# Kernel optimization log

Measured on AMD Instinct MI355X. Metric: run time of the kernel, lower is better.

The kernel has to match this reference:

```python
import jax, jax.numpy as jnp
import numpy as np

# Fixed production-scale dims (equal-size graphs -> no ragged padding needed)
B, NPG, C, H, L, FFN, NC = 16, 512, 128, 8, 4, 512, 4
D = C // H          # head dim = 16
T = NPG + 1         # +1 virtual graph token
EPG = 8192          # edges per graph (avg degree 16)
E = B * EPG


def _ln(x, g, b, eps=1e-5):
    m = x.mean(-1, keepdims=True)
    v = ((x - m) ** 2).mean(-1, keepdims=True)
    return (x - m) * jax.lax.rsqrt(v + eps) * g + b


def setup_inputs() -> dict:
    key = jax.random.key(0)
    ks = jax.random.split(key, 24)
    N = B * NPG
    node_feats = jax.random.normal(ks[0], (N, 3), jnp.float32)
    # intra-graph edges: local endpoints + per-graph node offset (matches batch_ptr math)
    local = jax.random.randint(ks[1], (2, B, EPG), 0, NPG)
    offs = (jnp.arange(B) * NPG)[None, :, None]
    edge_index = (local + offs).reshape(2, E)
    edge_attr = jax.random.randint(ks[2], (E,), 0, 10)

    def nrm(k, shape, scale=0.02):
        return jax.random.normal(k, shape, jnp.float32) * scale

    params = {
        "W_node": nrm(ks[3], (3, C), 0.3), "b_node": jnp.zeros((C,), jnp.float32),
        "graph_token": nrm(ks[4], (C,), 1.0),
        "edge_bias_table": nrm(ks[5], (11, H), 0.1).at[0].set(0.0),  # padding_idx=0
        "in_deg_emb": nrm(ks[6], (512, C)).at[0].set(0.0),           # padding_idx=0
        "out_deg_emb": nrm(ks[7], (512, C)).at[0].set(0.0),
        "vnode_bias": nrm(ks[8], (H,), 1.0),
        "Wq": nrm(ks[9], (L, C, C)), "bq": jnp.zeros((L, C), jnp.float32),
        "Wk": nrm(ks[10], (L, C, C)), "bk": jnp.zeros((L, C), jnp.float32),
        "Wv": nrm(ks[11], (L, C, C)), "bv": jnp.zeros((L, C), jnp.float32),
        "Wo": nrm(ks[12], (L, C, C)), "bo": jnp.zeros((L, C), jnp.float32),
        "ln1_g": jnp.ones((L, C), jnp.float32), "ln1_b": jnp.zeros((L, C), jnp.float32),
        "ln2_g": jnp.ones((L, C), jnp.float32), "ln2_b": jnp.zeros((L, C), jnp.float32),
        "W1": nrm(ks[13], (L, C, FFN)), "b1": jnp.zeros((L, FFN), jnp.float32),
        "W2": nrm(ks[14], (L, FFN, C)), "b2": jnp.zeros((L, C), jnp.float32),
        "normf_g": jnp.ones((C,), jnp.float32), "normf_b": jnp.zeros((C,), jnp.float32),
        "Wc1": nrm(ks[15], (C, C // 2)), "bc1": jnp.zeros((C // 2,), jnp.float32),
        "Wc2": nrm(ks[16], (C // 2, NC)), "bc2": jnp.zeros((NC,), jnp.float32),
    }
    return {"node_feats": node_feats, "edge_index": edge_index,
            "edge_attr": edge_attr, "num_graphs": B, **params}


def reference(node_feats, W_node, b_node, graph_token, edge_bias_table,
              in_deg_emb, out_deg_emb, vnode_bias,
              Wq, bq, Wk, bk, Wv, bv, Wo, bo,
              ln1_g, ln1_b, ln2_g, ln2_b, W1, b1, W2, b2,
              normf_g, normf_b, Wc1, bc1, Wc2, bc2,
              edge_index, edge_attr, num_graphs):
    N = node_feats.shape[0]
    npg = N // num_graphs
    t = npg + 1
    src, dst = edge_index[0], edge_index[1]
    # degree encoders (scatter_add of ones == segment_sum)
    in_deg = jnp.clip(jax.ops.segment_sum(jnp.ones_like(dst), dst, num_segments=N), 0, 511)
    out_deg = jnp.clip(jax.ops.segment_sum(jnp.ones_like(src), src, num_segments=N), 0, 511)
    x_enc = node_feats @ W_node + b_node + in_deg_emb[in_deg] + out_deg_emb[out_deg]
    # equal-size graphs with sorted batch ids -> padding loop is a reshape, mask all-False
    x = jnp.concatenate(
        [jnp.broadcast_to(graph_token, (num_graphs, 1, C)),
         x_enc.reshape(num_graphs, npg, C)], axis=1)  # [B, T, C]
    # attention bias: vnode row/col + scattered edge-attr embeddings
    bias = jnp.zeros((num_graphs, H, t, t), jnp.float32)
    bias = bias.at[:, :, 0, :].set(vnode_bias[None, :, None])
    bias = bias.at[:, :, :, 0].set(vnode_bias[None, :, None])
    eb = edge_bias_table[jnp.clip(edge_attr, 0, 9) + 1]  # [E, H]
    g = src // npg
    sl = src - g * npg + 1
    dl = dst - g * npg + 1
    bias = bias.at[g, :, sl, dl].add(eb)  # duplicate edges accumulate (scatter_add)
    scale = 1.0 / np.sqrt(D).astype(np.float32)
    for l in range(L):  # key_padding_mask is all-False here -> masked_fill is a no-op
        h = _ln(x, ln1_g[l], ln1_b[l])
        q = (h @ Wq[l] + bq[l]).reshape(num_graphs, t, H, D)
        k = (h @ Wk[l] + bk[l]).reshape(num_graphs, t, H, D)
        v = (h @ Wv[l] + bv[l]).reshape(num_graphs, t, H, D)
        scores = jnp.einsum('bthd,bshd->bhts', q, k) * scale + bias
        attn = jax.nn.softmax(scores, axis=-1)
        o = jnp.einsum('bhts,bshd->bthd', attn, v).reshape(num_graphs, t, C)
        x = x + o @ Wo[l] + bo[l]
        h2 = _ln(x, ln2_g[l], ln2_b[l])
        x = x + jax.nn.gelu(h2 @ W1[l] + b1[l], approximate=False) @ W2[l] + b2[l]
    x = _ln(x, normf_g, normf_b)
    gr = x[:, 0, :]  # virtual-node readout
    return jax.nn.gelu(gr @ Wc1 + bc1, approximate=False) @ Wc2 + bc2
```

## Files before the change

### kernel.cpp

```cpp
#include <hip/hip_runtime.h>
#include <hip/hip_bf16.h>

#define BB 16
#define NPG 512
#define CC 128
#define HH 8
#define LL 4
#define FFN 512
#define NCLS 4
#define DD 16
#define TT 513
#define EE 131072
#define NNODES 8192
#define ROWS (BB * TT)
#define ECAP 64
#define SP 544
#define BSTR 292

static constexpr size_t XROWS = (size_t)BB * TT;
static constexpr size_t XSZ   = XROWS * CC;
static constexpr size_t VTSZ  = (size_t)BB * HH * DD * SP;

typedef unsigned short ushort_t;
typedef __attribute__((ext_vector_type(8))) short short8;
typedef __attribute__((ext_vector_type(4))) float floatx4;

__device__ __forceinline__ float gelu_exact(float v) {
    return 0.5f * v * (1.0f + erff(v * 0.70710678118654752440f));
}
__device__ __forceinline__ ushort_t f2bf(float f) {
    union { float f; unsigned u; } c; c.f = f;
    unsigned u = c.u;
    return (ushort_t)((u + 0x7FFFu + ((u >> 16) & 1u)) >> 16);
}
__device__ __forceinline__ int swz(int row, int col, int stride) {
    int kb = col >> 3;
    return row * stride + (((kb ^ (row & 7)) << 3) | (col & 7));
}

__device__ __forceinline__ void qkv_stage(const ushort_t* hs,
                                          const ushort_t* Wtq, const float* bq_,
                                          const ushort_t* Wtk, const float* bk_,
                                          const ushort_t* Wtv, const float* bv_,
                                          ushort_t* qb, ushort_t* kb, ushort_t* vt,
                                          int m0, int wave, int lq, int quad) {
    const short* hsS = (const short*)hs;
    int n0 = wave * 32;
    int c0 = n0 + lq, c1 = n0 + 16 + lq;
    const short* Ws[3] = {(const short*)Wtq, (const short*)Wtk, (const short*)Wtv};
    const float* bs[3] = {bq_, bk_, bv_};
    size_t rB0 = (size_t)(n0 + lq) * CC, rB1 = (size_t)(n0 + 16 + lq) * CC;

    #pragma unroll
    for (int m = 0; m < 3; ++m) {
        const short* W = Ws[m];
        floatx4 a0 = {0.f,0.f,0.f,0.f}, a1 = a0;
        #pragma unroll
        for (int k0 = 0; k0 < CC; k0 += 32) {
            short8 af = *(const short8*)(hsS + swz(lq, k0 + quad * 8, 128));
            short8 b0 = *(const short8*)(W + rB0 + k0 + quad * 8);
            short8 b1 = *(const short8*)(W + rB1 + k0 + quad * 8);
            a0 = __builtin_amdgcn_mfma_f32_16x16x32_bf16(af, b0, a0, 0, 0, 0);
            a1 = __builtin_amdgcn_mfma_f32_16x16x32_bf16(af, b1, a1, 0, 0, 0);
        }
        float bv0 = bs[m][c0], bv1 = bs[m][c1];
        #pragma unroll
        for (int rg = 0; rg < 4; ++rg) {
            int r = m0 + quad * 4 + rg;
            float v0 = a0[rg] + bv0;
            float v1 = a1[rg] + bv1;
            if (m == 0) {
                qb[(size_t)r * CC + c0] = f2bf(v0 * 0.25f);
                qb[(size_t)r * CC + c1] = f2bf(v1 * 0.25f);
            } else if (m == 1) {
                kb[(size_t)r * CC + c0] = f2bf(v0);
                kb[(size_t)r * CC + c1] = f2bf(v1);
            } else {
                int bg = r / TT;
                int s = r - bg * TT;
                vt[((size_t)(bg * HH + (c0 >> 4)) * DD + (c0 & 15)) * SP + s] = f2bf(v0);
                vt[((size_t)(bg * HH + (c1 >> 4)) * DD + (c1 & 15)) * SP + s] = f2bf(v1);
            }
        }
    }
}

__global__ __launch_bounds__(256) void deg_csr_kernel(const int* __restrict__ ei,
                                                      const int* __restrict__ ea,
                                                      int* __restrict__ deg_in,
                                                      int* __restrict__ deg_out,
                                                      int* __restrict__ cnt,
                                                      int* __restrict__ ebuf) {
    int e = blockIdx.x * 256 + threadIdx.x;
    if (e >= EE) return;
    int src = ei[e], dst = ei[EE + e];
    atomicAdd(&deg_out[src], 1);
    atomicAdd(&deg_in[dst], 1);
    int g = src >> 9;
    int sl = src - (g << 9) + 1;
    int dl = dst - (g << 9) + 1;
    int a = ea[e];
    a = (a < 0) ? 0 : (a > 9 ? 9 : a);
    a += 1;
    int row = g * TT + sl;
    int pos = atomicAdd(&cnt[row], 1);
    if (pos < ECAP) ebuf[(size_t)row * ECAP + pos] = dl | (a << 16);
}

__global__ __launch_bounds__(256) void encode_kernel(const float* __restrict__ nf,
                                                     const float* __restrict__ Wn,
                                                     const float* __restrict__ bn,
                                                     const float* __restrict__ gt,
                                                     const float* __restrict__ ide,
                                                     const float* __restrict__ ode,
                                                     const int* __restrict__ deg_in,
                                                     const int* __restrict__ deg_out,
                                                     float* __restrict__ x) {
    int gid = blockIdx.x * 256 + threadIdx.x;
    if (gid >= (int)(XROWS * CC)) return;
    int c = gid & (CC - 1);
    int row = gid >> 7;
    int b = row / TT;
    int t = row - b * TT;
    float val;
    if (t == 0) {
        val = gt[c];
    } else {
        int i = b * NPG + t - 1;
        val = bn[c] + nf[i*3+0]*Wn[0*CC + c] + nf[i*3+1]*Wn[1*CC + c] + nf[i*3+2]*Wn[2*CC + c];
        int di = min(deg_in[i], 511);
        int dq = min(deg_out[i], 511);
        val += ide[(size_t)di * CC + c] + ode[(size_t)dq * CC + c];
    }
    x[(size_t)row * CC + c] = val;
}

struct TrDesc {
    const float* src[24];
    ushort_t*    dst[24];
    int          K[24];
    int          N[24];
};
__global__ __launch_bounds__(256) void tr_kernel(TrDesc d) {
    int z = blockIdx.z;
    int K = d.K[z], N = d.N[z];
    int tilesN = N >> 6;
    int ntile = (K >> 6) * tilesN;
    int tile = blockIdx.x;
    if (tile >= ntile) return;
    int k0 = (tile / tilesN) << 6;
    int n0 = (tile - (tile / tilesN) * tilesN) << 6;
    const float* src = d.src[z];
    ushort_t* dst = d.dst[z];
    __shared__ float t[64][65];
    int tid = threadIdx.x;
    int c = tid & 63, rb = tid >> 6;
    #pragma unroll
    for (int kk = 0; kk < 64; kk += 4)
        t[kk + rb][c] = src[(size_t)(k0 + kk + rb) * N + n0 + c];
    __syncthreads();
    #pragma unroll
    for (int nn = 0; nn < 64; nn += 4)
        dst[(size_t)(n0 + nn + rb) * K + k0 + c] = f2bf(t[c][nn + rb]);
}

__global__ __launch_bounds__(256) void pre_kernel(const float* __restrict__ x_,
                                                  const float* __restrict__ ln1g_,
                                                  const float* __restrict__ ln1b_,
                                                  const ushort_t* __restrict__ Wtq,
                                                  const float* __restrict__ bq_,
                                                  const ushort_t* __restrict__ Wtk,
                                                  const float* __restrict__ bk_,
                                                  const ushort_t* __restrict__ Wtv,
                                                  const float* __restrict__ bv_,
                                                  ushort_t* __restrict__ qb,
                                                  ushort_t* __restrict__ kb,
                                                  ushort_t* __restrict__ vt) {
    int m0 = blockIdx.x * 16;
    int tid = threadIdx.x;
    int wave = tid >> 6, lane = tid & 63, lq = lane & 15, quad = lane >> 4;

    __shared__ ushort_t hs[16 * 128];
    __shared__ float sred[4][16][2];

    int n0 = wave * 32;
    int c0 = n0 + lq, c1 = n0 + 16 + lq;
    float w0[4], w1[4];
    #pragma unroll
    for (int rg = 0; rg < 4; ++rg) {
        int r = m0 + quad * 4 + rg;
        w0[rg] = x_[(size_t)r * CC + c0];
        w1[rg] = x_[(size_t)r * CC + c1];
    }
    #pragma unroll
    for (int rg = 0; rg < 4; ++rg) {
        float s1 = w0[rg] + w1[rg];
        float s2 = w0[rg]*w0[rg] + w1[rg]*w1[rg];
        #pragma unroll
        for (int m = 1; m < 16; m <<= 1) {
            s1 += __shfl_xor(s1, m, 64);
            s2 += __shfl_xor(s2, m, 64);
        }
        if (lq == 0) { sred[wave][quad*4+rg][0] = s1; sred[wave][quad*4+rg][1] = s2; }
    }
    __syncthreads();
    float g0 = ln1g_[c0], g1 = ln1g_[c1], lb0 = ln1b_[c0], lb1 = ln1b_[c1];
    #pragma unroll
    for (int rg = 0; rg < 4; ++rg) {
        int row = quad * 4 + rg;
        float S1 = sred[0][row][0] + sred[1][row][0] + sred[2][row][0] + sred[3][row][0];
        float S2 = sred[0][row][1] + sred[1][row][1] + sred[2][row][1] + sred[3][row][1];
        float mn = S1 * (1.0f/CC);
        float var = S2 * (1.0f/CC) - mn * mn;
        float rs = rsqrtf(var + 1e-5f);
        hs[swz(row, c0, 128)] = f2bf((w0[rg] - mn) * rs * g0 + lb0);
        hs[swz(row, c1, 128)] = f2bf((w1[rg] - mn) * rs * g1 + lb1);
    }
    __syncthreads();
    qkv_stage(hs, Wtq, bq_, Wtk, bk_, Wtv, bv_, qb, kb, vt, m0, wave, lq, quad);
}

__global__ __launch_bounds__(256) void mega_kernel(const ushort_t* __restrict__ obf,
                                                   const ushort_t* __restrict__ WtO,
                                                   const float* __restrict__ bo_,
                                                   const float* __restrict__ ln2g_,
                                                   const float* __restrict__ ln2b_,
                                                   const ushort_t* __restrict__ Wt1_,
                                                   const float* __restrict__ b1_,
                                                   const ushort_t* __restrict__ Wt2_,
                                                   const float* __restrict__ b2_,
                                                   const float* __restrict__ ln1g_,
                                                   const float* __restrict__ ln1b_,
                                                   const ushort_t* __restrict__ Wtq,
                                                   const float* __restrict__ bq_,
                                                   const ushort_t* __restrict__ Wtk,
                                                   const float* __restrict__ bk_,
                                                   const ushort_t* __restrict__ Wtv,
                                                   const float* __restrict__ bv_,
                                                   float* __restrict__ x_,
                                                   ushort_t* __restrict__ qb,
                                                   ushort_t* __restrict__ kb,
                                                   ushort_t* __restrict__ vt,
                                                   int doQKV) {
    int m0 = blockIdx.x * 16;
    int tid = threadIdx.x;
    int wave = tid >> 6, lane = tid & 63, lq = lane & 15, quad = lane >> 4;

    __shared__ ushort_t hs[16 * 128];
    __shared__ ushort_t ms[16 * 512];
    __shared__ float sred[4][16][2];

    int n0 = wave * 32;
    int c0 = n0 + lq, c1 = n0 + 16 + lq;
    float vv0[4], vv1[4];

    {
        const short* Ab = (const short*)obf;
        const short* W = (const short*)WtO;
        size_t rowA = (size_t)(m0 + lq) * CC;
        size_t rB0 = (size_t)(n0 + lq) * CC, rB1 = (size_t)(n0 + 16 + lq) * CC;
        floatx4 a0 = {0.f,0.f,0.f,0.f}, a1 = a0;
        #pragma unroll
        for (int k0 = 0; k0 < CC; k0 += 32) {
            short8 af = *(const short8*)(Ab + rowA + k0 + quad * 8);
            short8 b0 = *(const short8*)(W + rB0 + k0 + quad * 8);
            short8 b1 = *(const short8*)(W + rB1 + k0 + quad * 8);
            a0 = __builtin_amdgcn_mfma_f32_16x16x32_bf16(af, b0, a0, 0, 0, 0);
            a1 = __builtin_amdgcn_mfma_f32_16x16x32_bf16(af, b1, a1, 0, 0, 0);
        }
        float bv0 = bo_[c0], bv1 = bo_[c1];
        #pragma unroll
        for (int rg = 0; rg < 4; ++rg) {
            int r = m0 + quad * 4 + rg;
            vv0[rg] = a0[rg] + bv0 + x_[(size_t)r * CC + c0];
            vv1[rg] = a1[rg] + bv1 + x_[(size_t)r * CC + c1];
        }
        #pragma unroll
        for (int rg = 0; rg < 4; ++rg) {
            float s1 = vv0[rg] + vv1[rg];
            float s2 = vv0[rg]*vv0[rg] + vv1[rg]*vv1[rg];
            #pragma unroll
            for (int m = 1; m < 16; m <<= 1) {
                s1 += __shfl_xor(s1, m, 64);
                s2 += __shfl_xor(s2, m, 64);
            }
            if (lq == 0) { sred[wave][quad*4+rg][0] = s1; sred[wave][quad*4+rg][1] = s2; }
        }
        __syncthreads();
        float g0 = ln2g_[c0], g1 = ln2g_[c1], lb0 = ln2b_[c0], lb1 = ln2b_[c1];
        #pragma unroll
        for (int rg = 0; rg < 4; ++rg) {
            int row = quad * 4 + rg;
            float S1 = sred[0][row][0] + sred[1][row][0] + sred[2][row][0] + sred[3][row][0];
            float S2 = sred[0][row][1] + sred[1][row][1] + sred[2][row][1] + sred[3][row][1];
            float mn = S1 * (1.0f/CC);
            float var = S2 * (1.0f/CC) - mn * mn;
            float rs = rsqrtf(var + 1e-5f);
            hs[swz(row, c0, 128)] = f2bf((vv0[rg] - mn) * rs * g0 + lb0);
            hs[swz(row, c1, 128)] = f2bf((vv1[rg] - mn) * rs * g1 + lb1);
        }
    }
    __syncthreads();

    {
        const short* hsS = (const short*)hs;
        const short* W = (const short*)Wt1_;
        #pragma unroll
        for (int nt = 0; nt < 4; ++nt) {
            int n = wave * 128 + nt * 32;
            size_t rB0 = (size_t)(n + lq) * CC, rB1 = (size_t)(n + 16 + lq) * CC;
            floatx4 a0 = {0.f,0.f,0.f,0.f}, a1 = a0;
            #pragma unroll
            for (int k0 = 0; k0 < CC; k0 += 32) {
                short8 af = *(const short8*)(hsS + swz(lq, k0 + quad * 8, 128));
                short8 b0 = *(const short8*)(W + rB0 + k0 + quad * 8);
                short8 b1 = *(const short8*)(W + rB1 + k0 + quad * 8);
                a0 = __builtin_amdgcn_mfma_f32_16x16x32_bf16(af, b0, a0, 0, 0, 0);
                a1 = __builtin_amdgcn_mfma_f32_16x16x32_bf16(af, b1, a1, 0, 0, 0);
            }
            float bb0 = b1_[n + lq], bb1 = b1_[n + 16 + lq];
            #pragma unroll
            for (int rg = 0; rg < 4; ++rg) {
                int row = quad * 4 + rg;
                ms[swz(row, n + lq, 512)]      = f2bf(gelu_exact(a0[rg] + bb0));
                ms[swz(row, n + 16 + lq, 512)] = f2bf(gelu_exact(a1[rg] + bb1));
            }
        }
    }
    __syncthreads();

    {
        const short* msS = (const short*)ms;
        const short* W = (const short*)Wt2_;
        size_t rB0 = (size_t)(n0 + lq) * FFN, rB1 = (size_t)(n0 + 16 + lq) * FFN;
        floatx4 a0 = {0.f,0.f,0.f,0.f}, a1 = a0;
        #pragma unroll 4
        for (int k0 = 0; k0 < FFN; k0 += 32) {
            short8 af = *(const short8*)(msS + swz(lq, k0 + quad * 8, 512));
            short8 b0 = *(const short8*)(W + rB0 + k0 + quad * 8);
            short8 b1 = *(const short8*)(W + rB1 + k0 + quad * 8);
            a0 = __builtin_amdgcn_mfma_f32_16x16x32_bf16(af, b0, a0, 0, 0, 0);
            a1 = __builtin_amdgcn_mfma_f32_16x16x32_bf16(af, b1, a1, 0, 0, 0);
        }
        float bv0 = b2_[c0], bv1 = b2_[c1];
        float w0[4], w1[4];
        #pragma unroll
        for (int rg = 0; rg < 4; ++rg) {
            int r = m0 + quad * 4 + rg;
            w0[rg] = a0[rg] + bv0 + vv0[rg];
            w1[rg] = a1[rg] + bv1 + vv1[rg];
            x_[(size_t)r * CC + c0] = w0[rg];
            x_[(size_t)r * CC + c1] = w1[rg];
        }
        if (!doQKV) return;
        #pragma unroll
        for (int rg = 0; rg < 4; ++rg) {
            float s1 = w0[rg] + w1[rg];
            float s2 = w0[rg]*w0[rg] + w1[rg]*w1[rg];
            #pragma unroll
            for (int m = 1; m < 16; m <<= 1) {
                s1 += __shfl_xor(s1, m, 64);
                s2 += __shfl_xor(s2, m, 64);
            }
            if (lq == 0) { sred[wave][quad*4+rg][0] = s1; sred[wave][quad*4+rg][1] = s2; }
        }
        __syncthreads();
        float g0 = ln1g_[c0], g1 = ln1g_[c1], lb0 = ln1b_[c0], lb1 = ln1b_[c1];
        #pragma unroll
        for (int rg = 0; rg < 4; ++rg) {
            int row = quad * 4 + rg;
            float S1 = sred[0][row][0] + sred[1][row][0] + sred[2][row][0] + sred[3][row][0];
            float S2 = sred[0][row][1] + sred[1][row][1] + sred[2][row][1] + sred[3][row][1];
            float mn = S1 * (1.0f/CC);
            float var = S2 * (1.0f/CC) - mn * mn;
            float rs = rsqrtf(var + 1e-5f);
            hs[swz(row, c0, 128)] = f2bf((w0[rg] - mn) * rs * g0 + lb0);
            hs[swz(row, c1, 128)] = f2bf((w1[rg] - mn) * rs * g1 + lb1);
        }
    }
    __syncthreads();

    qkv_stage(hs, Wtq, bq_, Wtk, bk_, Wtv, bv_, qb, kb, vt, m0, wave, lq, quad);
}

__global__ __launch_bounds__(256) void attn_kernel(const ushort_t* __restrict__ qb,
                                                   const ushort_t* __restrict__ kb,
                                                   const ushort_t* __restrict__ vt,
                                                   const int* __restrict__ cnt,
                                                   const int* __restrict__ ebuf,
                                                   const float* __restrict__ ebt,
                                                   const float* __restrict__ vnode,
                                                   ushort_t* __restrict__ ob) {
    int bh = blockIdx.x;
    int qt = blockIdx.y;
    int b = bh >> 3, h = bh & (HH - 1);
    int tid = threadIdx.x;
    int wave = tid >> 6, lane = tid & 63, lq = lane & 15, quad = lane >> 4;

    __shared__ float arena[16 * BSTR];
    float* bstrip = arena;

    int qg = qt * 16 + lq;
    int qr = qg < TT ? qg : TT - 1;
    short8 qf = {0,0,0,0,0,0,0,0};
    if (quad < 2)
        qf = *(const short8*)(qb + ((size_t)(b * TT + qr)) * CC + h * DD + quad * 8);
    float vbh = vnode[h];
    int ql = tid >> 4, e0 = tid & 15;
    int qs = qt * 16 + ql;
    int crow = b * TT + (qs < TT ? qs : 0);
    int cn = (qs > 0 && qs < TT) ? min(cnt[crow], ECAP) : 0;

    const short* kbS = (const short*)kb;
    const short* vtS = (const short*)(vt + (size_t)bh * DD * SP);

    floatx4 oacc = {0.f, 0.f, 0.f, 0.f};
    float lsum = 0.f;

    #pragma unroll
    for (int ch = 0; ch < 2; ++ch) {
        int sp_lo = ch ? 9 : 0;
        int sp_hi = ch ? 17 : 9;
        int s_lo  = ch ? 288 : 0;
        int nrows = ch ? 256 : 288;

        int sp = sp_lo + wave;
        short8 af0 = {0,0,0,0,0,0,0,0}, af1 = af0, vf = af0;
        if (sp < sp_hi) {
            int st0 = sp * 2, st1 = sp * 2 + 1;
            int kr0 = min(b * TT + st0 * 16 + lq, (int)XROWS - 1);
            int kr1 = min(b * TT + st1 * 16 + lq, (int)XROWS - 1);
            if (quad < 2) {
                af0 = *(const short8*)(kbS + (size_t)kr0 * CC + h * DD + quad * 8);
                af1 = *(const short8*)(kbS + (size_t)kr1 * CC + h * DD + quad * 8);
            }
            vf = *(const short8*)(vtS + (size_t)lq * SP + sp * 32 + quad * 8);
        }

        for (int i = tid; i < 16 * BSTR / 4; i += 256)
            ((float4*)bstrip)[i] = make_float4(0.f, 0.f, 0.f, 0.f);
        __syncthreads();
        if (ch == 0 && tid < 16) {
            int q = qt * 16 + tid;
            if (q > 0 && q < TT) bstrip[tid * BSTR] = vbh;
        }
        for (int j = e0; j < cn; j += 16) {
            int e = ebuf[(size_t)crow * ECAP + j];
            int dl = e & 0xFFFF, a = e >> 16;
            int loc = dl - s_lo;
            if (loc >= 0 && loc < nrows)
                atomicAdd(&bstrip[ql * BSTR + loc], ebt[a * 8 + h]);
        }
        __syncthreads();

        for (; sp < sp_hi; sp += 4) {
            int spn = sp + 4;
            short8 nf0 = {0,0,0,0,0,0,0,0}, nf1 = nf0, nvf = nf0;
            if (spn < sp_hi) {
                int st0 = spn * 2, st1 = spn * 2 + 1;
                int kr0 = min(b * TT + st0 * 16 + lq, (int)XROWS - 1);
                int kr1 = min(b * TT + st1 * 16 + lq, (int)XROWS - 1);
                if (quad < 2) {
                    nf0 = *(const short8*)(kbS + (size_t)kr0 * CC + h * DD + quad * 8);
                    nf1 = *(const short8*)(kbS + (size_t)kr1 * CC + h * DD + quad * 8);
                }
                nvf = *(const short8*)(vtS + (size_t)lq * SP + spn * 32 + quad * 8);
            }

            unsigned pw[2][2];
            #pragma unroll
            for (int t = 0; t < 2; ++t) {
                int st = sp * 2 + t;
                floatx4 c = __builtin_amdgcn_mfma_f32_16x16x32_bf16(
                    t ? af1 : af0, qf, (floatx4){0.f, 0.f, 0.f, 0.f}, 0, 0, 0);
                float4 bi = *(const float4*)(bstrip + lq * BSTR + (st * 16 - s_lo) + quad * 4);
                float biv[4] = {bi.x, bi.y, bi.z, bi.w};
                float pr[4];
                #pragma unroll
                for (int rg = 0; rg < 4; ++rg) {
                    int s = st * 16 + quad * 4 + rg;
                    float p = 0.f;
                    if (s < TT) p = __expf(c[rg] + biv[rg]);
                    lsum += p;
                    pr[rg] = p;
                }
                pw[t][0] = (unsigned)f2bf(pr[0]) | ((unsigned)f2bf(pr[1]) << 16);
                pw[t][1] = (unsigned)f2bf(pr[2]) | ((unsigned)f2bf(pr[3]) << 16);
            }
            int srcA = lq + (((2 * quad) & 3) << 4);
            int srcB = lq + (((2 * quad + 1) & 3) << 4);
            int a00 = __shfl((int)pw[0][0], srcA, 64);
            int a01 = __shfl((int)pw[0][1], srcA, 64);
            int a10 = __shfl((int)pw[1][0], srcA, 64);
            int a11 = __shfl((int)pw[1][1], srcA, 64);
            int b00 = __shfl((int)pw[0][0], srcB, 64);
            int b01 = __shfl((int)pw[0][1], srcB, 64);
            int b10 = __shfl((int)pw[1][0], srcB, 64);
            int b11 = __shfl((int)pw[1][1], srcB, 64);
            union { int u[4]; short8 s8; } pu;
            bool lo = quad < 2;
            pu.u[0] = lo ? a00 : a10;
            pu.u[1] = lo ? a01 : a11;
            pu.u[2] = lo ? b00 : b10;
            pu.u[3] = lo ? b01 : b11;
            oacc = __builtin_amdgcn_mfma_f32_16x16x32_bf16(vf, pu.s8, oacc, 0, 0, 0);

            af0 = nf0; af1 = nf1; vf = nvf;
        }
        __syncthreads();
    }

    lsum += __shfl_xor(lsum, 16, 64);
    lsum += __shfl_xor(lsum, 32, 64);
    float* redw = arena;
    float* lsumS = arena + 1088;
    #pragma unroll
    for (int rg = 0; rg < 4; ++rg)
        redw[wave * 272 + (quad * 4 + rg) * 17 + lq] = oacc[rg];
    if (quad == 0) lsumS[wave * 16 + lq] = lsum;
    __syncthreads();

    {
        int q = tid >> 4, d = tid & 15;
        float o = 0.f, L = 0.f;
        #pragma unroll
        for (int w = 0; w < 4; ++w) {
            o += redw[w * 272 + d * 17 + q];
            L += lsumS[w * 16 + q];
        }
        int qq = qt * 16 + q;
        if (qq < TT)
            ob[((size_t)(b * TT + qq)) * CC + h * DD + d] = f2bf(o / L);
    }
}

__global__ __launch_bounds__(128) void head_kernel(const float* __restrict__ x,
                                                   const float* __restrict__ ng,
                                                   const float* __restrict__ nb,
                                                   const float* __restrict__ Wc1,
                                                   const float* __restrict__ bc1,
                                                   const float* __restrict__ Wc2,
                                                   const float* __restrict__ bc2,
                                                   float* __restrict__ out) {
    int b = blockIdx.x;
    int c = threadIdx.x;
    __shared__ float xfs[CC];
    __shared__ float c1s[64];
    __shared__ float red[4];

    float v = x[((size_t)b * TT) * CC + c];
    float s1 = v, s2 = v * v;
    #pragma unroll
    for (int m = 32; m >= 1; m >>= 1) {
        s1 += __shfl_xor(s1, m, 64);
        s2 += __shfl_xor(s2, m, 64);
    }
    int w = c >> 6;
    if ((c & 63) == 0) { red[w*2] = s1; red[w*2+1] = s2; }
    __syncthreads();
    float S1 = red[0] + red[2], S2 = red[1] + red[3];
    float mn = S1 * (1.0f/CC);
    float var = S2 * (1.0f/CC) - mn * mn;
    float rs = rsqrtf(var + 1e-5f);
    xfs[c] = (v - mn) * rs * ng[c] + nb[c];
    __syncthreads();
    if (c < 64) {
        float a = bc1[c];
        #pragma unroll 4
        for (int k = 0; k < CC; ++k) a = fmaf(xfs[k], Wc1[(size_t)k * 64 + c], a);
        c1s[c] = gelu_exact(a);
    }
    __syncthreads();
    if (c < NCLS) {
        float a = bc2[c];
        #pragma unroll 4
        for (int j = 0; j < 64; ++j) a = fmaf(c1s[j], Wc2[(size_t)j * NCLS + c], a);
        out[(size_t)b * NCLS + c] = a;
    }
}

extern "C" void kernel_launch(void* const* d_in, const int* in_sizes, int n_in,
                              void* d_out, int out_size, void* d_ws, size_t ws_size,
                              hipStream_t stream) {
    const float* node_feats = (const float*)d_in[0];
    const int*   edge_index = (const int*)d_in[1];
    const int*   edge_attr  = (const int*)d_in[2];
    const float* W_node  = (const float*)d_in[4];
    const float* b_node  = (const float*)d_in[5];
    const float* g_token = (const float*)d_in[6];
    const float* ebt     = (const float*)d_in[7];
    const float* ide     = (const float*)d_in[8];
    const float* ode     = (const float*)d_in[9];
    const float* vnode   = (const float*)d_in[10];
    const float* Wq = (const float*)d_in[11];
    const float* bq = (const float*)d_in[12];
    const float* Wk = (const float*)d_in[13];
    const float* bk = (const float*)d_in[14];
    const float* Wv = (const float*)d_in[15];
    const float* bv = (const float*)d_in[16];
    const float* Wo = (const float*)d_in[17];
    const float* bo = (const float*)d_in[18];
    const float* ln1g = (const float*)d_in[19];
    const float* ln1b = (const float*)d_in[20];
    const float* ln2g = (const float*)d_in[21];
    const float* ln2b = (const float*)d_in[22];
    const float* W1 = (const float*)d_in[23];
    const float* b1 = (const float*)d_in[24];
    const float* W2 = (const float*)d_in[25];
    const float* b2 = (const float*)d_in[26];
    const float* nfg = (const float*)d_in[27];
    const float* nfb = (const float*)d_in[28];
    const float* Wc1 = (const float*)d_in[29];
    const float* bc1 = (const float*)d_in[30];
    const float* Wc2 = (const float*)d_in[31];
    const float* bc2 = (const float*)d_in[32];
    float* out = (float*)d_out;

    char* base = (char*)d_ws;
    float* x      = (float*)base;     base += XSZ * 4;
    ushort_t* qb  = (ushort_t*)base;  base += XSZ * 2;
    ushort_t* kb  = (ushort_t*)base;  base += XSZ * 2;
    ushort_t* vt  = (ushort_t*)base;  base += VTSZ * 2;
    ushort_t* obf = (ushort_t*)base;  base += XSZ * 2;
    ushort_t* wtqkvo = (ushort_t*)base; base += (size_t)16 * 16384 * 2;
    ushort_t* wt1 = (ushort_t*)base;  base += (size_t)4 * 65536 * 2;
    ushort_t* wt2 = (ushort_t*)base;  base += (size_t)4 * 65536 * 2;
    int* deg_in  = (int*)base;        base += NNODES * 4;
    int* deg_out = (int*)base;        base += NNODES * 4;
    int* cnt     = (int*)base;        base += (size_t)ROWS * 4;
    int* ebuf    = (int*)base;        base += (size_t)ROWS * ECAP * 4;

    hipMemsetAsync(deg_in, 0, (size_t)(2 * NNODES + ROWS) * 4, stream);
    deg_csr_kernel<<<EE / 256, 256, 0, stream>>>(edge_index, edge_attr,
                                                 deg_in, deg_out, cnt, ebuf);
    encode_kernel<<<(int)((XROWS * CC + 255) / 256), 256, 0, stream>>>(
        node_feats, W_node, b_node, g_token, ide, ode, deg_in, deg_out, x);

    TrDesc td;
    for (int l = 0; l < LL; ++l) {
        const float* srcs[4] = {Wq + (size_t)l*CC*CC, Wk + (size_t)l*CC*CC,
                                Wv + (size_t)l*CC*CC, Wo + (size_t)l*CC*CC};
        for (int k = 0; k < 4; ++k) {
            int slot = k * 4 + l;
            td.src[slot] = srcs[k];
            td.dst[slot] = wtqkvo + (size_t)slot * 16384;
            td.K[slot] = CC; td.N[slot] = CC;
        }
        td.src[16 + l] = W1 + (size_t)l*CC*FFN;
        td.dst[16 + l] = wt1 + (size_t)l*65536;
        td.K[16 + l] = CC; td.N[16 + l] = FFN;
        td.src[20 + l] = W2 + (size_t)l*FFN*CC;
        td.dst[20 + l] = wt2 + (size_t)l*65536;
        td.K[20 + l] = FFN; td.N[20 + l] = CC;
    }
    tr_kernel<<<dim3(16, 1, 24), 256, 0, stream>>>(td);

    const int MT16 = (int)(XROWS / 16);

    pre_kernel<<<MT16, 256, 0, stream>>>(
        x, ln1g, ln1b,
        wtqkvo + (size_t)(0*4+0)*16384, bq,
        wtqkvo + (size_t)(1*4+0)*16384, bk,
        wtqkvo + (size_t)(2*4+0)*16384, bv,
        qb, kb, vt);

    for (int l = 0; l < LL; ++l) {
        attn_kernel<<<dim3(BB*HH, 33), 256, 0, stream>>>(
            qb, kb, vt, cnt, ebuf, ebt, vnode, obf);

        int ln = (l + 1) % LL;
        mega_kernel<<<MT16, 256, 0, stream>>>(
            obf,
            wtqkvo + (size_t)(3*4+l)*16384, bo + l*CC,
            ln2g + l*CC, ln2b + l*CC,
            wt1 + (size_t)l*65536, b1 + l*FFN,
            wt2 + (size_t)l*65536, b2 + l*CC,
            ln1g + ln*CC, ln1b + ln*CC,
            wtqkvo + (size_t)(0*4+ln)*16384, bq + ln*CC,
            wtqkvo + (size_t)(1*4+ln)*16384, bk + ln*CC,
            wtqkvo + (size_t)(2*4+ln)*16384, bv + ln*CC,
            x, qb, kb, vt,
            (l < LL-1) ? 1 : 0);
    }

    head_kernel<<<BB, 128, 0, stream>>>(x, nfg, nfb, Wc1, bc1, Wc2, bc2, out);
}
```

Before: 436.0 us.

## Fuse setup kernels and classifier head into neighboring kernels to cut launches

Degree/CSR building and the weight transpose are merged into one launch split by block index. Node encoding is folded into the first LN+QKV kernel, so x no longer has to be written and then re-read. The classifier head moves into the final mega_kernel, where the block holding each graph's virtual-token row computes the output. This removes three kernel launches and one pass over x, at the cost of more code and heavier tail work in a few blocks of the last layer.

Measured after the change: 420.7 us. -3.5%, faster.

```diff
diff --git a/kernel.cpp b/kernel.cpp
--- a/kernel.cpp
+++ b/kernel.cpp
@@ -38,12 +38,12 @@
     return row * stride + (((kb ^ (row & 7)) << 3) | (col & 7));
 }
 
-__device__ __forceinline__ void qkv_stage(const ushort_t* hs,
-                                          const ushort_t* Wtq, const float* bq_,
-                                          const ushort_t* Wtk, const float* bk_,
-                                          const ushort_t* Wtv, const float* bv_,
-                                          ushort_t* qb, ushort_t* kb, ushort_t* vt,
-                                          int m0, int wave, int lq, int quad) {
+__device__ __forceinline__ void qkv_stage4(const ushort_t* hs,
+                                           const ushort_t* Wtq, const float* bq_,
+                                           const ushort_t* Wtk, const float* bk_,
+                                           const ushort_t* Wtv, const float* bv_,
+                                           ushort_t* qb, ushort_t* kb, ushort_t* vt,
+                                           int m0, int wave, int lq, int quad) {
     const short* hsS = (const short*)hs;
     int n0 = wave * 32;
     int c0 = n0 + lq, c1 = n0 + 16 + lq;
@@ -85,75 +85,63 @@
     }
 }
 
-__global__ __launch_bounds__(256) void deg_csr_kernel(const int* __restrict__ ei,
-                                                      const int* __restrict__ ea,
-                                                      int* __restrict__ deg_in,
-                                                      int* __restrict__ deg_out,
-                                                      int* __restrict__ cnt,
-                                                      int* __restrict__ ebuf) {
-    int e = blockIdx.x * 256 + threadIdx.x;
-    if (e >= EE) return;
-    int src = ei[e], dst = ei[EE + e];
-    atomicAdd(&deg_out[src], 1);
-    atomicAdd(&deg_in[dst], 1);
-    int g = src >> 9;
-    int sl = src - (g << 9) + 1;
-    int dl = dst - (g << 9) + 1;
-    int a = ea[e];
-    a = (a < 0) ? 0 : (a > 9 ? 9 : a);
-    a += 1;
-    int row = g * TT + sl;
-    int pos = atomicAdd(&cnt[row], 1);
-    if (pos < ECAP) ebuf[(size_t)row * ECAP + pos] = dl | (a << 16);
-}
-
-__global__ __launch_bounds__(256) void encode_kernel(const float* __restrict__ nf,
-                                                     const float* __restrict__ Wn,
-                                                     const float* __restrict__ bn,
-                                                     const float* __restrict__ gt,
-                                                     const float* __restrict__ ide,
-                                                     const float* __restrict__ ode,
-                                                     const int* __restrict__ deg_in,
-                                                     const int* __restrict__ deg_out,
-                                                     float* __restrict__ x) {
-    int gid = blockIdx.x * 256 + threadIdx.x;
-    if (gid >= (int)(XROWS * CC)) return;
-    int c = gid & (CC - 1);
-    int row = gid >> 7;
-    int b = row / TT;
-    int t = row - b * TT;
-    float val;
-    if (t == 0) {
-        val = gt[c];
+__global__ __launch_bounds__(256) void deg_csr_tr_kernel(const int* __restrict__ ei,
+                                                         const int* __restrict__ ea,
+                                                         int* __restrict__ deg_in,
+                                                         int* __restrict__ deg_out,
+                                                         int* __restrict__ cnt,
+                                                         int* __restrict__ ebuf,
+                                                         const float* __restrict__ Wq,
+                                                         const float* __restrict__ Wk,
+                                                         const float* __restrict__ Wv,
+                                                         const float* __restrict__ Wo,
+                                                         const float* __restrict__ W1,
+                                                         const float* __restrict__ W2,
+                                                         ushort_t* __restrict__ wtqkvo,
+                                                         ushort_t* __restrict__ wt1,
+                                                         ushort_t* __restrict__ wt2) {
+    int bid = blockIdx.x;
+    int tid = threadIdx.x;
+    if (bid < 512) {
+        int e = bid * 256 + tid;
+        int src = ei[e], dst = ei[EE + e];
+        atomicAdd(&deg_out[src], 1);
+        atomicAdd(&deg_in[dst], 1);
+        int g = src >> 9;
+        int sl = src - (g << 9) + 1;
+        int dl = dst - (g << 9) + 1;
+        int a = ea[e];
+        a = (a < 0) ? 0 : (a > 9 ? 9 : a);
+        a += 1;
+        int row = g * TT + sl;
+        int pos = atomicAdd(&cnt[row], 1);
+        if (pos < ECAP) ebuf[(size_t)row * ECAP + pos] = dl | (a << 16);
+        return;
+    }
+    int z = bid - 512;
+    const float* src; ushort_t* dst; int K, N, tile;
+    if (z < 64) {
+        int zz = z >> 2; tile = z & 3;
+        int k = zz >> 2, l = zz & 3;
+        const float* s4[4] = {Wq, Wk, Wv, Wo};
+        src = s4[k] + (size_t)l * CC * CC;
+        dst = wtqkvo + (size_t)(k * 4 + l) * 16384;
+        K = CC; N = CC;
+    } else if (z < 128) {
+        int l = (z - 64) >> 4; tile = (z - 64) & 15;
+        src = W1 + (size_t)l * CC * FFN;
+        dst = wt1 + (size_t)l * 65536;
+        K = CC; N = FFN;
     } else {
-        int i = b * NPG + t - 1;
-        val = bn[c] + nf[i*3+0]*Wn[0*CC + c] + nf[i*3+1]*Wn[1*CC + c] + nf[i*3+2]*Wn[2*CC + c];
-        int di = min(deg_in[i], 511);
-        int dq = min(deg_out[i], 511);
-        val += ide[(size_t)di * CC + c] + ode[(size_t)dq * CC + c];
-    }
-    x[(size_t)row * CC + c] = val;
-}
-
-struct TrDesc {
-    const float* src[24];
-    ushort_t*    dst[24];
-    int          K[24];
-    int          N[24];
-};
-__global__ __launch_bounds__(256) void tr_kernel(TrDesc d) {
-    int z = blockIdx.z;
-    int K = d.K[z], N = d.N[z];
+        int l = (z - 128) >> 4; tile = (z - 128) & 15;
+        src = W2 + (size_t)l * FFN * CC;
+        dst = wt2 + (size_t)l * 65536;
+        K = FFN; N = CC;
+    }
     int tilesN = N >> 6;
-    int ntile = (K >> 6) * tilesN;
-    int tile = blockIdx.x;
-    if (tile >= ntile) return;
     int k0 = (tile / tilesN) << 6;
     int n0 = (tile - (tile / tilesN) * tilesN) << 6;
-    const float* src = d.src[z];
-    ushort_t* dst = d.dst[z];
     __shared__ float t[64][65];
-    int tid = threadIdx.x;
     int c = tid & 63, rb = tid >> 6;
     #pragma unroll
     for (int kk = 0; kk < 64; kk += 4)
@@ -164,18 +152,24 @@
         dst[(size_t)(n0 + nn + rb) * K + k0 + c] = f2bf(t[c][nn + rb]);
 }
 
-__global__ __launch_bounds__(256) void pre_kernel(const float* __restrict__ x_,
-                                                  const float* __restrict__ ln1g_,
-                                                  const float* __restrict__ ln1b_,
-                                                  const ushort_t* __restrict__ Wtq,
-                                                  const float* __restrict__ bq_,
-                                                  const ushort_t* __restrict__ Wtk,
-                                                  const float* __restrict__ bk_,
-                                                  const ushort_t* __restrict__ Wtv,
-                                                  const float* __restrict__ bv_,
-                                                  ushort_t* __restrict__ qb,
-                                                  ushort_t* __restrict__ kb,
-                                                  ushort_t* __restrict__ vt) {
+__global__ __launch_bounds__(256) void encode_pre_kernel(const float* __restrict__ nf,
+                                                         const float* __restrict__ Wn,
+                                                         const float* __restrict__ bn,
+                                                         const float* __restrict__ gt,
+                                                         const float* __restrict__ ide,
+                                                         const float* __restrict__ ode,
+                                                         const int* __restrict__ deg_in,
+                                                         const int* __restrict__ deg_out,
+                                                         const float* __restrict__ ln1g_,
+                                                         const float* __restrict__ ln1b_,
+                                                         const ushort_t* __restrict__ wtqkvo,
+                                                         const float* __restrict__ bq_,
+                                                         const float* __restrict__ bk_,
+                                                         const float* __restrict__ bv_,
+                                                         float* __restrict__ x_,
+                                                         ushort_t* __restrict__ qb,
+                                                         ushort_t* __restrict__ kb,
+                                                         ushort_t* __restrict__ vt) {
     int m0 = blockIdx.x * 16;
     int tid = threadIdx.x;
     int wave = tid >> 6, lane = tid & 63, lq = lane & 15, quad = lane >> 4;
@@ -189,8 +183,24 @@
     #pragma unroll
     for (int rg = 0; rg < 4; ++rg) {
         int r = m0 + quad * 4 + rg;
-        w0[rg] = x_[(size_t)r * CC + c0];
-        w1[rg] = x_[(size_t)r * CC + c1];
+        int b = r / TT;
+        int t = r - b * TT;
+        float v0, v1;
+        if (t == 0) {
+            v0 = gt[c0]; v1 = gt[c1];
+        } else {
+            int i = b * NPG + t - 1;
+            float f0 = nf[i*3+0], f1 = nf[i*3+1], f2 = nf[i*3+2];
+            v0 = bn[c0] + f0*Wn[0*CC + c0] + f1*Wn[1*CC + c0] + f2*Wn[2*CC + c0];
+            v1 = bn[c1] + f0*Wn[0*CC + c1] + f1*Wn[1*CC + c1] + f2*Wn[2*CC + c1];
+            int di = min(deg_in[i], 511);
+            int dq = min(deg_out[i], 511);
+            v0 += ide[(size_t)di * CC + c0] + ode[(size_t)dq * CC + c0];
+            v1 += ide[(size_t)di * CC + c1] + ode[(size_t)dq * CC + c1];
+        }
+        x_[(size_t)r * CC + c0] = v0;
+        x_[(size_t)r * CC + c1] = v1;
+        w0[rg] = v0; w1[rg] = v1;
     }
     #pragma unroll
     for (int rg = 0; rg < 4; ++rg) {
@@ -217,7 +227,10 @@
         hs[swz(row, c1, 128)] = f2bf((w1[rg] - mn) * rs * g1 + lb1);
     }
     __syncthreads();
-    qkv_stage(hs, Wtq, bq_, Wtk, bk_, Wtv, bv_, qb, kb, vt, m0, wave, lq, quad);
+    qkv_stage4(hs, wtqkvo, bq_,
+               wtqkvo + (size_t)4 * 16384, bk_,
+               wtqkvo + (size_t)8 * 16384, bv_,
+               qb, kb, vt, m0, wave, lq, quad);
 }
 
 __global__ __launch_bounds__(256) void mega_kernel(const ushort_t* __restrict__ obf,
@@ -237,10 +250,17 @@
                                                    const float* __restrict__ bk_,
                                                    const ushort_t* __restrict__ Wtv,
                                                    const float* __restrict__ bv_,
+                                                   const float* __restrict__ nfg,
+                                                   const float* __restrict__ nfb,
+                                                   const float* __restrict__ Wc1,
+                                                   const float* __restrict__ bc1,
+                                                   const float* __restrict__ Wc2,
+                                                   const float* __restrict__ bc2,
                                                    float* __restrict__ x_,
                                                    ushort_t* __restrict__ qb,
                                                    ushort_t* __restrict__ kb,
                                                    ushort_t* __restrict__ vt,
+                                                   float* __restrict__ out,
                                                    int doQKV) {
     int m0 = blockIdx.x * 16;
     int tid = threadIdx.x;
@@ -329,6 +349,7 @@
     }
     __syncthreads();
 
+    float w0[4], w1[4];
     {
         const short* msS = (const short*)ms;
         const short* W = (const short*)Wt2_;
@@ -343,7 +364,6 @@
             a1 = __builtin_amdgcn_mfma_f32_16x16x32_bf16(af, b1, a1, 0, 0, 0);
         }
         float bv0 = b2_[c0], bv1 = b2_[c1];
-        float w0[4], w1[4];
         #pragma unroll
         for (int rg = 0; rg < 4; ++rg) {
             int r = m0 + quad * 4 + rg;
@@ -352,7 +372,9 @@
             x_[(size_t)r * CC + c0] = w0[rg];
             x_[(size_t)r * CC + c1] = w1[rg];
         }
-        if (!doQKV) return;
+    }
+
+    if (doQKV) {
         #pragma unroll
         for (int rg = 0; rg < 4; ++rg) {
             float s1 = w0[rg] + w1[rg];
@@ -377,10 +399,61 @@
             hs[swz(row, c0, 128)] = f2bf((w0[rg] - mn) * rs * g0 + lb0);
             hs[swz(row, c1, 128)] = f2bf((w1[rg] - mn) * rs * g1 + lb1);
         }
-    }
-    __syncthreads();
-
-    qkv_stage(hs, Wtq, bq_, Wtk, bk_, Wtv, bv_, qb, kb, vt, m0, wave, lq, quad);
+        __syncthreads();
+        qkv_stage4(hs, Wtq, bq_, Wtk, bk_, Wtv, bv_, qb, kb, vt, m0, wave, lq, quad);
+        return;
+    }
+
+    int gb = (m0 + TT - 1) / TT;
+    int rgt = gb * TT;
+    if (gb >= BB || rgt >= m0 + 16) return;
+    int hb = rgt - m0;
+
+    __syncthreads();
+    float* hrow = (float*)ms;
+    float* xfs  = hrow + CC;
+    float* c1s  = xfs + CC;
+    float* red  = c1s + 64;
+    #pragma unroll
+    for (int rg = 0; rg < 4; ++rg) {
+        if (quad * 4 + rg == hb) { hrow[c0] = w0[rg]; hrow[c1] = w1[rg]; }
+    }
+    __syncthreads();
+
+    {
+        int c = tid;
+        float v = 0.f, s1 = 0.f, s2 = 0.f;
+        if (c < CC) { v = hrow[c]; s1 = v; s2 = v * v; }
+        #pragma unroll
+        for (int m = 32; m >= 1; m >>= 1) {
+            s1 += __shfl_xor(s1, m, 64);
+            s2 += __shfl_xor(s2, m, 64);
+        }
+        int w = c >> 6;
+        if (c < CC && (c & 63) == 0) { red[w*2] = s1; red[w*2+1] = s2; }
+        __syncthreads();
+        if (c < CC) {
+            float S1 = red[0] + red[2], S2 = red[1] + red[3];
+            float mn = S1 * (1.0f/CC);
+            float var = S2 * (1.0f/CC) - mn * mn;
+            float rs = rsqrtf(var + 1e-5f);
+            xfs[c] = (v - mn) * rs * nfg[c] + nfb[c];
+        }
+        __syncthreads();
+        if (c < 64) {
+            float acc = bc1[c];
+            #pragma unroll 4
+            for (int k = 0; k < CC; ++k) acc = fmaf(xfs[k], Wc1[(size_t)k * 64 + c], acc);
+            c1s[c] = gelu_exact(acc);
+        }
+        __syncthreads();
+        if (c < NCLS) {
+            float acc = bc2[c];
+            #pragma unroll 4
+            for (int j = 0; j < 64; ++j) acc = fmaf(c1s[j], Wc2[(size_t)j * NCLS + c], acc);
+            out[(size_t)gb * NCLS + c] = acc;
+        }
+    }
 }
 
 __global__ __launch_bounds__(256) void attn_kernel(const ushort_t* __restrict__ qb,
@@ -531,51 +604,6 @@
         int qq = qt * 16 + q;
         if (qq < TT)
             ob[((size_t)(b * TT + qq)) * CC + h * DD + d] = f2bf(o / L);
-    }
-}
-
-__global__ __launch_bounds__(128) void head_kernel(const float* __restrict__ x,
-                                                   const float* __restrict__ ng,
-                                                   const float* __restrict__ nb,
-                                                   const float* __restrict__ Wc1,
-                                                   const float* __restrict__ bc1,
-                                                   const float* __restrict__ Wc2,
-                                                   const float* __restrict__ bc2,
-                                                   float* __restrict__ out) {
-    int b = blockIdx.x;
-    int c = threadIdx.x;
-    __shared__ float xfs[CC];
-    __shared__ float c1s[64];
-    __shared__ float red[4];
-
-    float v = x[((size_t)b * TT) * CC + c];
-    float s1 = v, s2 = v * v;
-    #pragma unroll
-    for (int m = 32; m >= 1; m >>= 1) {
-        s1 += __shfl_xor(s1, m, 64);
-        s2 += __shfl_xor(s2, m, 64);
-    }
-    int w = c >> 6;
-    if ((c & 63) == 0) { red[w*2] = s1; red[w*2+1] = s2; }
-    __syncthreads();
-    float S1 = red[0] + red[2], S2 = red[1] + red[3];
-    float mn = S1 * (1.0f/CC);
-    float var = S2 * (1.0f/CC) - mn * mn;
-    float rs = rsqrtf(var + 1e-5f);
-    xfs[c] = (v - mn) * rs * ng[c] + nb[c];
-    __syncthreads();
-    if (c < 64) {
-        float a = bc1[c];
-        #pragma unroll 4
-        for (int k = 0; k < CC; ++k) a = fmaf(xfs[k], Wc1[(size_t)k * 64 + c], a);
-        c1s[c] = gelu_exact(a);
-    }
-    __syncthreads();
-    if (c < NCLS) {
-        float a = bc2[c];
-        #pragma unroll 4
-        for (int j = 0; j < 64; ++j) a = fmaf(c1s[j], Wc2[(size_t)j * NCLS + c], a);
-        out[(size_t)b * NCLS + c] = a;
     }
 }
 
@@ -630,39 +658,16 @@
     int* cnt     = (int*)base;        base += (size_t)ROWS * 4;
     int* ebuf    = (int*)base;        base += (size_t)ROWS * ECAP * 4;
 
+    const int MT16 = (int)(XROWS / 16);
+
     hipMemsetAsync(deg_in, 0, (size_t)(2 * NNODES + ROWS) * 4, stream);
-    deg_csr_kernel<<<EE / 256, 256, 0, stream>>>(edge_index, edge_attr,
-                                                 deg_in, deg_out, cnt, ebuf);
-    encode_kernel<<<(int)((XROWS * CC + 255) / 256), 256, 0, stream>>>(
-        node_feats, W_node, b_node, g_token, ide, ode, deg_in, deg_out, x);
-
-    TrDesc td;
-    for (int l = 0; l < LL; ++l) {
-        const float* srcs[4] = {Wq + (size_t)l*CC*CC, Wk + (size_t)l*CC*CC,
-                                Wv + (size_t)l*CC*CC, Wo + (size_t)l*CC*CC};
-        for (int k = 0; k < 4; ++k) {
-            int slot = k * 4 + l;
-            td.src[slot] = srcs[k];
-            td.dst[slot] = wtqkvo + (size_t)slot * 16384;
-            td.K[slot] = CC; td.N[slot] = CC;
-        }
-        td.src[16 + l] = W1 + (size_t)l*CC*FFN;
-        td.dst[16 + l] = wt1 + (size_t)l*65536;
-        td.K[16 + l] = CC; td.N[16 + l] = FFN;
-        td.src[20 + l] = W2 + (size_t)l*FFN*CC;
-        td.dst[20 + l] = wt2 + (size_t)l*65536;
-        td.K[20 + l] = FFN; td.N[20 + l] = CC;
-    }
-    tr_kernel<<<dim3(16, 1, 24), 256, 0, stream>>>(td);
-
-    const int MT16 = (int)(XROWS / 16);
-
-    pre_kernel<<<MT16, 256, 0, stream>>>(
-        x, ln1g, ln1b,
-        wtqkvo + (size_t)(0*4+0)*16384, bq,
-        wtqkvo + (size_t)(1*4+0)*16384, bk,
-        wtqkvo + (size_t)(2*4+0)*16384, bv,
-        qb, kb, vt);
+    deg_csr_tr_kernel<<<512 + 192, 256, 0, stream>>>(
+        edge_index, edge_attr, deg_in, deg_out, cnt, ebuf,
+        Wq, Wk, Wv, Wo, W1, W2, wtqkvo, wt1, wt2);
+
+    encode_pre_kernel<<<MT16, 256, 0, stream>>>(
+        node_feats, W_node, b_node, g_token, ide, ode, deg_in, deg_out,
+        ln1g, ln1b, wtqkvo, bq, bk, bv, x, qb, kb, vt);
 
     for (int l = 0; l < LL; ++l) {
         attn_kernel<<<dim3(BB*HH, 33), 256, 0, stream>>>(
@@ -671,17 +676,16 @@
         int ln = (l + 1) % LL;
         mega_kernel<<<MT16, 256, 0, stream>>>(
             obf,
-            wtqkvo + (size_t)(3*4+l)*16384, bo + l*CC,
+            wtqkvo + (size_t)(12 + l)*16384, bo + l*CC,
             ln2g + l*CC, ln2b + l*CC,
             wt1 + (size_t)l*65536, b1 + l*FFN,
             wt2 + (size_t)l*65536, b2 + l*CC,
             ln1g + ln*CC, ln1b + ln*CC,
-            wtqkvo + (size_t)(0*4+ln)*16384, bq + ln*CC,
-            wtqkvo + (size_t)(1*4+ln)*16384, bk + ln*CC,
-            wtqkvo + (size_t)(2*4+ln)*16384, bv + ln*CC,
-            x, qb, kb, vt,
+            wtqkvo + (size_t)(0 + ln)*16384, bq + ln*CC,
+            wtqkvo + (size_t)(4 + ln)*16384, bk + ln*CC,
+            wtqkvo + (size_t)(8 + ln)*16384, bv + ln*CC,
+            nfg, nfb, Wc1, bc1, Wc2, bc2,
+            x, qb, kb, vt, out,
             (l < LL-1) ? 1 : 0);
     }
-
-    head_kernel<<<BB, 128, 0, stream>>>(x, nfg, nfb, Wc1, bc1, Wc2, bc2, out);
-}
+}
```
